# Kernel optimization log

Hardware: AMD Instinct MI355X
Metric: run time of the kernel (lower is better)

## Reference

```python
import jax, jax.numpy as jnp
import numpy as np

T, H, I = 4096, 4096, 11008  # tokens, hidden_size, intermediate_size
QMAX = 127.0


def setup_inputs() -> dict:
    key = jax.random.key(0)
    k0, k1, k2, k3, k4 = jax.random.split(key, 5)
    x = jax.random.normal(k0, (T, H), dtype=jnp.float32)
    # int8 weights stored as float32 integer values in [-127, 127]
    wq_gate_up = jnp.round(jnp.clip(jax.random.normal(k1, (2 * I, H), dtype=jnp.float32) * 30.0, -QMAX, QMAX))
    s_gate_up = jax.random.uniform(k2, (2 * I,), dtype=jnp.float32, minval=5e-4, maxval=2e-3)
    wq_down = jnp.round(jnp.clip(jax.random.normal(k3, (H, I), dtype=jnp.float32) * 30.0, -QMAX, QMAX))
    s_down = jax.random.uniform(k4, (H,), dtype=jnp.float32, minval=5e-4, maxval=2e-3)
    return {"x": x, "wq_gate_up": wq_gate_up, "s_gate_up": s_gate_up,
            "wq_down": wq_down, "s_down": s_down}


def reference(x, wq_gate_up, s_gate_up, wq_down, s_down):
    # --- quantize activations (per-tensor dynamic int8) ---
    x_scale = jnp.max(jnp.abs(x)) / QMAX
    qx = jnp.clip(jnp.round(x / x_scale), -QMAX, QMAX)  # integer-valued f32 (simulated int8)

    # --- gate_up_proj: int8 GEMM (int32 accumulate simulated in f32) ---
    acc = qx @ wq_gate_up.T                             # [T, 2I]
    gate_up = acc * (x_scale * s_gate_up)               # dequant: per-tensor act * per-channel weight scale

    # --- DequantSiluAndMulQuant: silu(gate) * up, then dynamic requant ---
    gate, up = jnp.split(gate_up, 2, axis=-1)           # [T, I] each
    h = jax.nn.silu(gate) * up
    h_scale = jnp.max(jnp.abs(h)) / QMAX
    qh = jnp.clip(jnp.round(h / h_scale), -QMAX, QMAX)

    # --- down_proj: int8 GEMM + dequant ---
    out = (qh @ wq_down.T) * (h_scale * s_down)         # [T, H]
    return out, h_scale
```

## Files before the change

kernel.cpp:

```cpp
#include <hip/hip_runtime.h>

#define T_DIM 4096
#define K1    4096
#define I_DIM 11008
#define QMAXF 127.0f

typedef int v4i  __attribute__((ext_vector_type(4)));
typedef int v16i __attribute__((ext_vector_type(16)));


__device__ __forceinline__ void gload16(const void* g, void* l) {
  __builtin_amdgcn_global_load_lds((__attribute__((address_space(1))) unsigned int*)(g),
                                   (__attribute__((address_space(3))) unsigned int*)(l),
                                   16, 0, 0);
}

__device__ __forceinline__ int packq(float a, float b, float c, float d) {
  return ((int)a & 255) | (((int)b & 255) << 8) | (((int)c & 255) << 16) | (((int)d & 255) << 24);
}

#define MFMA32(A, B, C) __builtin_amdgcn_mfma_i32_32x32x32_i8(A, B, C, 0, 0, 0)


__global__ void absmax_x_kernel(const float4* __restrict__ x4, unsigned* __restrict__ maxbits, int n4) {
  int tid = blockIdx.x * blockDim.x + threadIdx.x;
  int stride = gridDim.x * blockDim.x;
  float m = 0.f;
  for (int i = tid; i < n4; i += stride) {
    float4 v = x4[i];
    m = fmaxf(m, fmaxf(fmaxf(fabsf(v.x), fabsf(v.y)), fmaxf(fabsf(v.z), fabsf(v.w))));
  }
  #pragma unroll
  for (int off = 32; off; off >>= 1) m = fmaxf(m, __shfl_xor(m, off));
  if ((threadIdx.x & 63) == 0) atomicMax(maxbits, __float_as_uint(m));
}


__global__ void quant_x_kernel(const float4* __restrict__ x4, v4i* __restrict__ q4,
                               const unsigned* __restrict__ scal) {
  const float sx = __uint_as_float(scal[0]) * (1.0f / QMAXF);
  const long i = (long)blockIdx.x * blockDim.x + threadIdx.x;
  v4i o;
  #pragma unroll
  for (int j = 0; j < 4; ++j) {
    float4 v = x4[i * 4 + j];
    float a = fminf(fmaxf(rintf(v.x / sx), -QMAXF), QMAXF);
    float b = fminf(fmaxf(rintf(v.y / sx), -QMAXF), QMAXF);
    float c = fminf(fmaxf(rintf(v.z / sx), -QMAXF), QMAXF);
    float d = fminf(fmaxf(rintf(v.w / sx), -QMAXF), QMAXF);
    o[j] = packq(a, b, c, d);
  }
  q4[i] = o;
}


__global__ void conv_w_kernel(const float4* __restrict__ w4, v4i* __restrict__ q4) {
  const long i = (long)blockIdx.x * blockDim.x + threadIdx.x;
  v4i o;
  #pragma unroll
  for (int j = 0; j < 4; ++j) {
    float4 v = w4[i * 4 + j];
    o[j] = packq(rintf(v.x), rintf(v.y), rintf(v.z), rintf(v.w));
  }
  q4[i] = o;
}


#define STG2(KO, SB) {                                                      \
    gload16(gAs + (KO),      &L[SB][lA]);                                   \
    gload16(gAs + (KO) + 32, &L[SB][lA + 8192]);                            \
    gload16(gBs + (KO),      &L[SB][lB]);                                   \
    gload16(gBs + (KO) + 32, &L[SB][lB + 8192]);                            \
  }

#define WBODY(U)                                                            \
  {                                                                         \
    const signed char* Lb = L[(U)];                                         \
    v4i a0 = *(const v4i*)&Lb[kgl * 4096 + ab];                             \
    v4i a1 = *(const v4i*)&Lb[kgl * 4096 + ab + 512];                       \
    v4i b0 = *(const v4i*)&Lb[kgl * 4096 + bb];                             \
    v4i b1 = *(const v4i*)&Lb[kgl * 4096 + bb + 512];                       \
    v4i b2 = *(const v4i*)&Lb[kgl * 4096 + bb + 1024];                      \
    v4i b3 = *(const v4i*)&Lb[kgl * 4096 + bb + 1536];                      \
    v4i a2 = *(const v4i*)&Lb[(2 + kgl) * 4096 + ab];                       \
    v4i a3 = *(const v4i*)&Lb[(2 + kgl) * 4096 + ab + 512];                 \
    v4i b4 = *(const v4i*)&Lb[(2 + kgl) * 4096 + bb];                       \
    v4i b5 = *(const v4i*)&Lb[(2 + kgl) * 4096 + bb + 512];                 \
    v4i b6 = *(const v4i*)&Lb[(2 + kgl) * 4096 + bb + 1024];                \
    v4i b7 = *(const v4i*)&Lb[(2 + kgl) * 4096 + bb + 1536];                \
    acc[0][0] = MFMA32(a0, b0, acc[0][0]);                                  \
    acc[0][1] = MFMA32(a0, b1, acc[0][1]);                                  \
    acc[0][2] = MFMA32(a0, b2, acc[0][2]);                                  \
    acc[0][3] = MFMA32(a0, b3, acc[0][3]);                                  \
    acc[1][0] = MFMA32(a1, b0, acc[1][0]);                                  \
    acc[1][1] = MFMA32(a1, b1, acc[1][1]);                                  \
    acc[1][2] = MFMA32(a1, b2, acc[1][2]);                                  \
    acc[1][3] = MFMA32(a1, b3, acc[1][3]);                                  \
    acc[0][0] = MFMA32(a2, b4, acc[0][0]);                                  \
    acc[0][1] = MFMA32(a2, b5, acc[0][1]);                                  \
    acc[0][2] = MFMA32(a2, b6, acc[0][2]);                                  \
    acc[0][3] = MFMA32(a2, b7, acc[0][3]);                                  \
    acc[1][0] = MFMA32(a3, b4, acc[1][0]);                                  \
    acc[1][1] = MFMA32(a3, b5, acc[1][1]);                                  \
    acc[1][2] = MFMA32(a3, b6, acc[1][2]);                                  \
    acc[1][3] = MFMA32(a3, b7, acc[1][3]);                                  \
  }

#define WINDOW(U0, U1, S0, S1, KO0, KO1, DS0, DS1)                          \
  {                                                                         \
    asm volatile("s_waitcnt vmcnt(0)" ::: "memory");                        \
    __builtin_amdgcn_s_barrier();                                           \
    asm volatile("" ::: "memory");                                          \
    if (DS0) STG2(KO0, S0);                                                 \
    if (DS1) STG2(KO1, S1);                                                 \
    WBODY(U0)                                                               \
    WBODY(U1)                                                               \
  }


__global__ __launch_bounds__(512, 2)
void gemm1_silu_kernel(const signed char* __restrict__ qx,
                       const signed char* __restrict__ w8,
                       const float* __restrict__ sgu,
                       unsigned* __restrict__ scal,
                       float* __restrict__ hbuf)
{
  __shared__ signed char L[4][32768];

  const int tid  = threadIdx.x;
  const int lane = tid & 63;
  const int wid  = tid >> 6;
  const int wr   = wid >> 1;
  const int wc   = wid & 1;
  const int l31  = lane & 31;
  const int kgl  = lane >> 5;

  const int lin = blockIdx.x;
  const int sw  = (lin & 7) * 172 + (lin >> 3);
  const int brow = (sw & 15) * 256;
  const int bcol = (sw >> 4) * 128;

  const int sr = tid & 255, sk = tid >> 8;
  const signed char* gA = qx + (size_t)(brow + sr) * K1 + sk * 16;
  const int grp = sr >> 6, w = sr & 63;
  const int gcolw = bcol + grp * 32 + (w & 31);
  const size_t srcrow = (w < 32) ? (size_t)gcolw : (size_t)(I_DIM + gcolw);
  const signed char* gB = w8 + srcrow * K1 + sk * 16;
  const int lA = tid * 16;
  const int lB = 16384 + tid * 16;

  const int ab = (wr * 64 + l31) * 16;
  const int bb = 16384 + (wc * 128 + l31) * 16;

  v16i zero = {0};
  v16i acc[2][4];
  #pragma unroll
  for (int m = 0; m < 2; ++m)
    #pragma unroll
    for (int n = 0; n < 4; ++n) acc[m][n] = zero;

  const signed char* gAs = gA;
  const signed char* gBs = gB;

  STG2(0, 0);
  STG2(64, 1);

  for (int p = 0; p < 15; ++p) {
    WINDOW(0, 1, 2, 3, 128, 192, 1, 1)
    WINDOW(2, 3, 0, 1, 256, 320, 1, 1)
    gAs += 256; gBs += 256;
  }
  WINDOW(0, 1, 2, 3, 128, 192, 1, 1)
  WINDOW(2, 3, 0, 1, 0, 0, 0, 0)

  const float xsc = __uint_as_float(scal[0]) * (1.0f / QMAXF);
  float hmax = 0.f;
  #pragma unroll
  for (int m = 0; m < 2; ++m) {
    const int rbase = brow + wr * 64 + m * 32 + 4 * kgl;
    #pragma unroll
    for (int p = 0; p < 2; ++p) {
      const int col = bcol + (wc * 2 + p) * 32 + l31;
      const float sg = sgu[col] * xsc;
      const float su = sgu[I_DIM + col] * xsc;
      #pragma unroll
      for (int q = 0; q < 16; ++q) {
        const int row = rbase + (q & 3) + 8 * (q >> 2);
        float g = (float)acc[m][2 * p][q] * sg;
        float u = (float)acc[m][2 * p + 1][q] * su;
        float hv = (g / (1.f + expf(-g))) * u;
        hmax = fmaxf(hmax, fabsf(hv));
        hbuf[(size_t)row * I_DIM + col] = hv;
      }
    }
  }
  #pragma unroll
  for (int off = 32; off; off >>= 1) hmax = fmaxf(hmax, __shfl_xor(hmax, off));
  if (lane == 0) atomicMax(scal + 1, __float_as_uint(hmax));
}


__global__ void quant_h_kernel(const float4* __restrict__ h4, v4i* __restrict__ q4,
                               const unsigned* __restrict__ scal, float* __restrict__ hs_out) {
  const float hs = __uint_as_float(scal[1]) * (1.0f / QMAXF);
  const long i = (long)blockIdx.x * blockDim.x + threadIdx.x;
  if (i == 0) hs_out[0] = hs;
  v4i o;
  #pragma unroll
  for (int j = 0; j < 4; ++j) {
    float4 v = h4[i * 4 + j];
    float a = fminf(fmaxf(rintf(v.x / hs), -QMAXF), QMAXF);
    float b = fminf(fmaxf(rintf(v.y / hs), -QMAXF), QMAXF);
    float c = fminf(fmaxf(rintf(v.z / hs), -QMAXF), QMAXF);
    float d = fminf(fmaxf(rintf(v.w / hs), -QMAXF), QMAXF);
    o[j] = packq(a, b, c, d);
  }
  q4[i] = o;
}


__global__ __launch_bounds__(512, 2)
void gemm2_kernel(const signed char* __restrict__ qh,
                  const signed char* __restrict__ w8,
                  const float* __restrict__ sdn,
                  const unsigned* __restrict__ scal,
                  float* __restrict__ out)
{
  __shared__ signed char L[4][32768];

  const int tid  = threadIdx.x;
  const int lane = tid & 63;
  const int wid  = tid >> 6;
  const int wr   = wid >> 1;
  const int wc   = wid & 1;
  const int l31  = lane & 31;
  const int kgl  = lane >> 5;

  const int lin = blockIdx.x;
  const int sw  = (lin & 7) * 32 + (lin >> 3);
  const int brow = (sw & 15) * 256;
  const int bcol = (sw >> 4) * 256;

  const int sr = tid & 255, sk = tid >> 8;
  const signed char* gA = qh + (size_t)(brow + sr) * I_DIM + sk * 16;
  const signed char* gB = w8 + (size_t)(bcol + sr) * I_DIM + sk * 16;
  const int lA = tid * 16;
  const int lB = 16384 + tid * 16;

  const int ab = (wr * 64 + l31) * 16;
  const int bb = 16384 + (wc * 128 + l31) * 16;

  v16i zero = {0};
  v16i acc[2][4];
  #pragma unroll
  for (int m = 0; m < 2; ++m)
    #pragma unroll
    for (int n = 0; n < 4; ++n) acc[m][n] = zero;

  const signed char* gAs = gA;
  const signed char* gBs = gB;

  STG2(0, 0);
  STG2(64, 1);

  for (int p = 0; p < 42; ++p) {
    WINDOW(0, 1, 2, 3, 128, 192, 1, 1)
    WINDOW(2, 3, 0, 1, 256, 320, 1, 1)
    gAs += 256; gBs += 256;
  }
  WINDOW(0, 1, 2, 3, 128, 192, 1, 1)
  WINDOW(2, 3, 0, 1, 0, 0, 0, 0)

  const float hsc = __uint_as_float(scal[1]) * (1.0f / QMAXF);
  #pragma unroll
  for (int m = 0; m < 2; ++m) {
    const int rbase = brow + wr * 64 + m * 32 + 4 * kgl;
    #pragma unroll
    for (int n = 0; n < 4; ++n) {
      const int col = bcol + wc * 128 + n * 32 + l31;
      const float s = sdn[col] * hsc;
      #pragma unroll
      for (int q = 0; q < 16; ++q) {
        const int row = rbase + (q & 3) + 8 * (q >> 2);
        out[(size_t)row * K1 + col] = (float)acc[m][n][q] * s;
      }
    }
  }
}


extern "C" void kernel_launch(void* const* d_in, const int* in_sizes, int n_in,
                              void* d_out, int out_size, void* d_ws, size_t ws_size,
                              hipStream_t stream) {
  (void)in_sizes; (void)n_in; (void)out_size; (void)ws_size;
  const float* x   = (const float*)d_in[0];
  const float* wgu = (const float*)d_in[1];
  const float* sgu = (const float*)d_in[2];
  const float* wdn = (const float*)d_in[3];
  const float* sdn = (const float*)d_in[4];
  float* out = (float*)d_out;
  char* ws = (char*)d_ws;

  signed char* qx  = (signed char*)(ws + 0LL);
  signed char* w8g = (signed char*)(ws + 16777216LL);
  signed char* w8d = (signed char*)(ws + 106954752LL);
  signed char* qh  = (signed char*)(ws + 152043520LL);
  float*       hb  = (float*)      (ws + 197132288LL);
  unsigned*    scal= (unsigned*)   (ws + 377487360LL);

  hipMemsetAsync(scal, 0, 256, stream);
  absmax_x_kernel<<<2048, 256, 0, stream>>>((const float4*)x, scal, T_DIM * K1 / 4);
  quant_x_kernel<<<4096, 256, 0, stream>>>((const float4*)x, (v4i*)qx, scal);
  conv_w_kernel<<<22016, 256, 0, stream>>>((const float4*)wgu, (v4i*)w8g);
  conv_w_kernel<<<11008, 256, 0, stream>>>((const float4*)wdn, (v4i*)w8d);

  gemm1_silu_kernel<<<1376, 512, 0, stream>>>(qx, w8g, sgu, scal, hb);

  quant_h_kernel<<<11008, 256, 0, stream>>>((const float4*)hb, (v4i*)qh, scal,
                                            out + (size_t)T_DIM * K1);

  gemm2_kernel<<<256, 512, 0, stream>>>(qh, w8d, sdn, scal, out);
}
```

Measured before the change: 1.331 ms.

## Shrink GEMM block tiles to 128 rows with triple-buffered LDS pipeline

Both int8 GEMMs drop from 256-row block tiles to 128-row tiles, with 8 waves arranged 2x4 and each wave holding four accumulators instead of eight. The LDS ring goes from four 32 KB stages to three 24 KB stages, and the wait changes from vmcnt(0) to vmcnt(3) so one stage stays in flight while another is consumed. Launch bounds rise to 4 blocks per CU and the grids double. The aim is more resident waves and better load/compute overlap, and gemm2 in particular gets more blocks than CUs. The cost is less operand reuse per block, so more global/L2 traffic per FLOP.

```diff
diff --git a/kernel.cpp b/kernel.cpp
--- a/kernel.cpp
+++ b/kernel.cpp
@@ -66,132 +66,107 @@
 }
 
 
-#define STG2(KO, SB) {                                                      \
-    gload16(gAs + (KO),      &L[SB][lA]);                                   \
-    gload16(gAs + (KO) + 32, &L[SB][lA + 8192]);                            \
-    gload16(gBs + (KO),      &L[SB][lB]);                                   \
-    gload16(gBs + (KO) + 32, &L[SB][lB + 8192]);                            \
-  }
-
-#define WBODY(U)                                                            \
+#define STG3(KO, SB) {                                                      \
+    gload16(gA1 + (KO),      &L[SB][lA]);                                   \
+    gload16(gB1 + (KO),      &L[SB][lB]);                                   \
+    gload16(gB1 + (KO) + 32, &L[SB][lB + 8192]);                            \
+  }
+
+#define TILE(U, SB, KO, DOST, VM)                                           \
   {                                                                         \
+    asm volatile("s_waitcnt vmcnt(" VM ")" ::: "memory");                   \
+    __builtin_amdgcn_s_barrier();                                           \
+    asm volatile("" ::: "memory");                                          \
+    if (DOST) STG3(KO, SB);                                                 \
     const signed char* Lb = L[(U)];                                         \
-    v4i a0 = *(const v4i*)&Lb[kgl * 4096 + ab];                             \
-    v4i a1 = *(const v4i*)&Lb[kgl * 4096 + ab + 512];                       \
+    v4i a0 = *(const v4i*)&Lb[kgl * 2048 + ab];                             \
+    v4i a1 = *(const v4i*)&Lb[kgl * 2048 + ab + 512];                       \
     v4i b0 = *(const v4i*)&Lb[kgl * 4096 + bb];                             \
     v4i b1 = *(const v4i*)&Lb[kgl * 4096 + bb + 512];                       \
-    v4i b2 = *(const v4i*)&Lb[kgl * 4096 + bb + 1024];                      \
-    v4i b3 = *(const v4i*)&Lb[kgl * 4096 + bb + 1536];                      \
-    v4i a2 = *(const v4i*)&Lb[(2 + kgl) * 4096 + ab];                       \
-    v4i a3 = *(const v4i*)&Lb[(2 + kgl) * 4096 + ab + 512];                 \
-    v4i b4 = *(const v4i*)&Lb[(2 + kgl) * 4096 + bb];                       \
-    v4i b5 = *(const v4i*)&Lb[(2 + kgl) * 4096 + bb + 512];                 \
-    v4i b6 = *(const v4i*)&Lb[(2 + kgl) * 4096 + bb + 1024];                \
-    v4i b7 = *(const v4i*)&Lb[(2 + kgl) * 4096 + bb + 1536];                \
-    acc[0][0] = MFMA32(a0, b0, acc[0][0]);                                  \
-    acc[0][1] = MFMA32(a0, b1, acc[0][1]);                                  \
-    acc[0][2] = MFMA32(a0, b2, acc[0][2]);                                  \
-    acc[0][3] = MFMA32(a0, b3, acc[0][3]);                                  \
-    acc[1][0] = MFMA32(a1, b0, acc[1][0]);                                  \
-    acc[1][1] = MFMA32(a1, b1, acc[1][1]);                                  \
-    acc[1][2] = MFMA32(a1, b2, acc[1][2]);                                  \
-    acc[1][3] = MFMA32(a1, b3, acc[1][3]);                                  \
-    acc[0][0] = MFMA32(a2, b4, acc[0][0]);                                  \
-    acc[0][1] = MFMA32(a2, b5, acc[0][1]);                                  \
-    acc[0][2] = MFMA32(a2, b6, acc[0][2]);                                  \
-    acc[0][3] = MFMA32(a2, b7, acc[0][3]);                                  \
-    acc[1][0] = MFMA32(a3, b4, acc[1][0]);                                  \
-    acc[1][1] = MFMA32(a3, b5, acc[1][1]);                                  \
-    acc[1][2] = MFMA32(a3, b6, acc[1][2]);                                  \
-    acc[1][3] = MFMA32(a3, b7, acc[1][3]);                                  \
-  }
-
-#define WINDOW(U0, U1, S0, S1, KO0, KO1, DS0, DS1)                          \
-  {                                                                         \
-    asm volatile("s_waitcnt vmcnt(0)" ::: "memory");                        \
-    __builtin_amdgcn_s_barrier();                                           \
-    asm volatile("" ::: "memory");                                          \
-    if (DS0) STG2(KO0, S0);                                                 \
-    if (DS1) STG2(KO1, S1);                                                 \
-    WBODY(U0)                                                               \
-    WBODY(U1)                                                               \
-  }
-
-
-__global__ __launch_bounds__(512, 2)
+    v4i a2 = *(const v4i*)&Lb[(2 + kgl) * 2048 + ab];                       \
+    v4i a3 = *(const v4i*)&Lb[(2 + kgl) * 2048 + ab + 512];                 \
+    v4i b2 = *(const v4i*)&Lb[(2 + kgl) * 4096 + bb];                       \
+    v4i b3 = *(const v4i*)&Lb[(2 + kgl) * 4096 + bb + 512];                 \
+    acc00 = MFMA32(a0, b0, acc00);                                          \
+    acc01 = MFMA32(a0, b1, acc01);                                          \
+    acc10 = MFMA32(a1, b0, acc10);                                          \
+    acc11 = MFMA32(a1, b1, acc11);                                          \
+    acc00 = MFMA32(a2, b2, acc00);                                          \
+    acc01 = MFMA32(a2, b3, acc01);                                          \
+    acc10 = MFMA32(a3, b2, acc10);                                          \
+    acc11 = MFMA32(a3, b3, acc11);                                          \
+  }
+
+
+__global__ __launch_bounds__(512, 4)
 void gemm1_silu_kernel(const signed char* __restrict__ qx,
                        const signed char* __restrict__ w8,
                        const float* __restrict__ sgu,
                        unsigned* __restrict__ scal,
                        float* __restrict__ hbuf)
 {
-  __shared__ signed char L[4][32768];
+  __shared__ signed char L[3][24576];
 
   const int tid  = threadIdx.x;
   const int lane = tid & 63;
   const int wid  = tid >> 6;
-  const int wr   = wid >> 1;
-  const int wc   = wid & 1;
+  const int wr   = wid >> 2;
+  const int wc   = wid & 3;
   const int l31  = lane & 31;
   const int kgl  = lane >> 5;
 
   const int lin = blockIdx.x;
-  const int sw  = (lin & 7) * 172 + (lin >> 3);
-  const int brow = (sw & 15) * 256;
-  const int bcol = (sw >> 4) * 128;
-
+  const int sw  = (lin & 7) * 344 + (lin >> 3);
+  const int brow = (sw & 31) * 128;
+  const int bcol = (sw >> 5) * 128;
+
+  const int sra = tid & 127, ska = tid >> 7;
+  const signed char* gA1 = qx + (size_t)(brow + sra) * K1 + ska * 16;
   const int sr = tid & 255, sk = tid >> 8;
-  const signed char* gA = qx + (size_t)(brow + sr) * K1 + sk * 16;
   const int grp = sr >> 6, w = sr & 63;
   const int gcolw = bcol + grp * 32 + (w & 31);
   const size_t srcrow = (w < 32) ? (size_t)gcolw : (size_t)(I_DIM + gcolw);
-  const signed char* gB = w8 + srcrow * K1 + sk * 16;
+  const signed char* gB1 = w8 + srcrow * K1 + sk * 16;
   const int lA = tid * 16;
-  const int lB = 16384 + tid * 16;
+  const int lB = 8192 + tid * 16;
 
   const int ab = (wr * 64 + l31) * 16;
-  const int bb = 16384 + (wc * 128 + l31) * 16;
-
-  v16i zero = {0};
-  v16i acc[2][4];
-  #pragma unroll
-  for (int m = 0; m < 2; ++m)
-    #pragma unroll
-    for (int n = 0; n < 4; ++n) acc[m][n] = zero;
-
-  const signed char* gAs = gA;
-  const signed char* gBs = gB;
-
-  STG2(0, 0);
-  STG2(64, 1);
-
-  for (int p = 0; p < 15; ++p) {
-    WINDOW(0, 1, 2, 3, 128, 192, 1, 1)
-    WINDOW(2, 3, 0, 1, 256, 320, 1, 1)
-    gAs += 256; gBs += 256;
-  }
-  WINDOW(0, 1, 2, 3, 128, 192, 1, 1)
-  WINDOW(2, 3, 0, 1, 0, 0, 0, 0)
+  const int bb = 8192 + (wc * 64 + l31) * 16;
+
+  v16i acc00 = {0}, acc01 = {0}, acc10 = {0}, acc11 = {0};
+
+  STG3(0, 0);
+  STG3(64, 1);
+
+  for (int p = 0; p < 20; ++p) {
+    TILE(0, 2, 128, 1, "3")
+    TILE(1, 0, 192, 1, "3")
+    TILE(2, 1, 256, 1, "3")
+    gA1 += 192; gB1 += 192;
+  }
+  TILE(0, 2, 128, 1, "3")
+  TILE(1, 0, 192, 1, "3")
+  TILE(2, 0, 0,   0, "3")
+  TILE(0, 0, 0,   0, "0")
 
   const float xsc = __uint_as_float(scal[0]) * (1.0f / QMAXF);
+  const int col = bcol + wc * 32 + l31;
+  const float sg = sgu[col] * xsc;
+  const float su = sgu[I_DIM + col] * xsc;
   float hmax = 0.f;
   #pragma unroll
   for (int m = 0; m < 2; ++m) {
     const int rbase = brow + wr * 64 + m * 32 + 4 * kgl;
+    const v16i ag = m ? acc10 : acc00;
+    const v16i au = m ? acc11 : acc01;
     #pragma unroll
-    for (int p = 0; p < 2; ++p) {
-      const int col = bcol + (wc * 2 + p) * 32 + l31;
-      const float sg = sgu[col] * xsc;
-      const float su = sgu[I_DIM + col] * xsc;
-      #pragma unroll
-      for (int q = 0; q < 16; ++q) {
-        const int row = rbase + (q & 3) + 8 * (q >> 2);
-        float g = (float)acc[m][2 * p][q] * sg;
-        float u = (float)acc[m][2 * p + 1][q] * su;
-        float hv = (g / (1.f + expf(-g))) * u;
-        hmax = fmaxf(hmax, fabsf(hv));
-        hbuf[(size_t)row * I_DIM + col] = hv;
-      }
+    for (int q = 0; q < 16; ++q) {
+      const int row = rbase + (q & 3) + 8 * (q >> 2);
+      float g = (float)ag[q] * sg;
+      float u = (float)au[q] * su;
+      float hv = (g / (1.f + expf(-g))) * u;
+      hmax = fmaxf(hmax, fabsf(hv));
+      hbuf[(size_t)row * I_DIM + col] = hv;
     }
   }
   #pragma unroll
@@ -219,70 +194,67 @@
 }
 
 
-__global__ __launch_bounds__(512, 2)
+__global__ __launch_bounds__(512, 4)
 void gemm2_kernel(const signed char* __restrict__ qh,
                   const signed char* __restrict__ w8,
                   const float* __restrict__ sdn,
                   const unsigned* __restrict__ scal,
                   float* __restrict__ out)
 {
-  __shared__ signed char L[4][32768];
+  __shared__ signed char L[3][24576];
 
   const int tid  = threadIdx.x;
   const int lane = tid & 63;
   const int wid  = tid >> 6;
-  const int wr   = wid >> 1;
-  const int wc   = wid & 1;
+  const int wr   = wid >> 2;
+  const int wc   = wid & 3;
   const int l31  = lane & 31;
   const int kgl  = lane >> 5;
 
   const int lin = blockIdx.x;
-  const int sw  = (lin & 7) * 32 + (lin >> 3);
-  const int brow = (sw & 15) * 256;
-  const int bcol = (sw >> 4) * 256;
-
+  const int sw  = (lin & 7) * 64 + (lin >> 3);
+  const int brow = (sw & 31) * 128;
+  const int bcol = (sw >> 5) * 256;
+
+  const int sra = tid & 127, ska = tid >> 7;
+  const signed char* gA1 = qh + (size_t)(brow + sra) * I_DIM + ska * 16;
   const int sr = tid & 255, sk = tid >> 8;
-  const signed char* gA = qh + (size_t)(brow + sr) * I_DIM + sk * 16;
-  const signed char* gB = w8 + (size_t)(bcol + sr) * I_DIM + sk * 16;
+  const signed char* gB1 = w8 + (size_t)(bcol + sr) * I_DIM + sk * 16;
   const int lA = tid * 16;
-  const int lB = 16384 + tid * 16;
+  const int lB = 8192 + tid * 16;
 
   const int ab = (wr * 64 + l31) * 16;
-  const int bb = 16384 + (wc * 128 + l31) * 16;
-
-  v16i zero = {0};
-  v16i acc[2][4];
-  #pragma unroll
-  for (int m = 0; m < 2; ++m)
-    #pragma unroll
-    for (int n = 0; n < 4; ++n) acc[m][n] = zero;
-
-  const signed char* gAs = gA;
-  const signed char* gBs = gB;
-
-  STG2(0, 0);
-  STG2(64, 1);
-
-  for (int p = 0; p < 42; ++p) {
-    WINDOW(0, 1, 2, 3, 128, 192, 1, 1)
-    WINDOW(2, 3, 0, 1, 256, 320, 1, 1)
-    gAs += 256; gBs += 256;
-  }
-  WINDOW(0, 1, 2, 3, 128, 192, 1, 1)
-  WINDOW(2, 3, 0, 1, 0, 0, 0, 0)
+  const int bb = 8192 + (wc * 64 + l31) * 16;
+
+  v16i acc00 = {0}, acc01 = {0}, acc10 = {0}, acc11 = {0};
+
+  STG3(0, 0);
+  STG3(64, 1);
+
+  for (int p = 0; p < 56; ++p) {
+    TILE(0, 2, 128, 1, "3")
+    TILE(1, 0, 192, 1, "3")
+    TILE(2, 1, 256, 1, "3")
+    gA1 += 192; gB1 += 192;
+  }
+  TILE(0, 2, 128, 1, "3")
+  TILE(1, 0, 192, 1, "3")
+  TILE(2, 0, 0,   0, "3")
+  TILE(0, 0, 0,   0, "0")
 
   const float hsc = __uint_as_float(scal[1]) * (1.0f / QMAXF);
   #pragma unroll
   for (int m = 0; m < 2; ++m) {
     const int rbase = brow + wr * 64 + m * 32 + 4 * kgl;
     #pragma unroll
-    for (int n = 0; n < 4; ++n) {
-      const int col = bcol + wc * 128 + n * 32 + l31;
+    for (int n = 0; n < 2; ++n) {
+      const int col = bcol + wc * 64 + n * 32 + l31;
       const float s = sdn[col] * hsc;
+      const v16i av = m ? (n ? acc11 : acc10) : (n ? acc01 : acc00);
       #pragma unroll
       for (int q = 0; q < 16; ++q) {
         const int row = rbase + (q & 3) + 8 * (q >> 2);
-        out[(size_t)row * K1 + col] = (float)acc[m][n][q] * s;
+        out[(size_t)row * K1 + col] = (float)av[q] * s;
       }
     }
   }
@@ -314,10 +286,10 @@
   conv_w_kernel<<<22016, 256, 0, stream>>>((const float4*)wgu, (v4i*)w8g);
   conv_w_kernel<<<11008, 256, 0, stream>>>((const float4*)wdn, (v4i*)w8d);
 
-  gemm1_silu_kernel<<<1376, 512, 0, stream>>>(qx, w8g, sgu, scal, hb);
+  gemm1_silu_kernel<<<2752, 512, 0, stream>>>(qx, w8g, sgu, scal, hb);
 
   quant_h_kernel<<<11008, 256, 0, stream>>>((const float4*)hb, (v4i*)qh, scal,
                                             out + (size_t)T_DIM * K1);
 
-  gemm2_kernel<<<256, 512, 0, stream>>>(qh, w8d, sdn, scal, out);
-}
+  gemm2_kernel<<<512, 512, 0, stream>>>(qh, w8d, sdn, scal, out);
+}
```

New measurement: 1.535 ms. 15.4% more time.

## Restructure int8 GEMM main loops into double-buffered two-phase pipeline with priority hints

Applied to the files above, without the earlier changes.

Both GEMM kernels replace the four-slot 64-wide K staging with two 128-wide K buffers, so each iteration has one vmcnt wait and barrier instead of two. Each iteration is split into two phases: LDS fragments are read first, then the A half or B half of the next tile is issued, then a barrier and lgkmcnt wait precede the MFMA burst. The MFMA burst is raised with s_setprio and fenced by sched_barrier. The aim is to interleave global-to-LDS loads with matrix math and cut synchronisation overhead. The trade-off is a shallower prefetch depth (one tile ahead), which may expose memory latency.

```diff
diff --git a/kernel.cpp b/kernel.cpp
--- a/kernel.cpp
+++ b/kernel.cpp
@@ -66,55 +66,68 @@
 }
 
 
-#define STG2(KO, SB) {                                                      \
-    gload16(gAs + (KO),      &L[SB][lA]);                                   \
-    gload16(gAs + (KO) + 32, &L[SB][lA + 8192]);                            \
-    gload16(gBs + (KO),      &L[SB][lB]);                                   \
-    gload16(gBs + (KO) + 32, &L[SB][lB + 8192]);                            \
-  }
-
-#define WBODY(U)                                                            \
+#define STG_A4(KO, LS) {                                                    \
+    gload16(gA + (KO),      &LS[lA]);                                       \
+    gload16(gA + (KO) + 32, &LS[lA + 8192]);                                \
+    gload16(gA + (KO) + 64, &LS[lA + 16384]);                               \
+    gload16(gA + (KO) + 96, &LS[lA + 24576]);                               \
+  }
+#define STG_B4(KO, LS) {                                                    \
+    gload16(gB + (KO),      &LS[lB]);                                       \
+    gload16(gB + (KO) + 32, &LS[lB + 8192]);                                \
+    gload16(gB + (KO) + 64, &LS[lB + 16384]);                               \
+    gload16(gB + (KO) + 96, &LS[lB + 24576]);                               \
+  }
+
+#define PHASE(KS0, STMT_STAGE)                                              \
   {                                                                         \
-    const signed char* Lb = L[(U)];                                         \
-    v4i a0 = *(const v4i*)&Lb[kgl * 4096 + ab];                             \
-    v4i a1 = *(const v4i*)&Lb[kgl * 4096 + ab + 512];                       \
-    v4i b0 = *(const v4i*)&Lb[kgl * 4096 + bb];                             \
-    v4i b1 = *(const v4i*)&Lb[kgl * 4096 + bb + 512];                       \
-    v4i b2 = *(const v4i*)&Lb[kgl * 4096 + bb + 1024];                      \
-    v4i b3 = *(const v4i*)&Lb[kgl * 4096 + bb + 1536];                      \
-    v4i a2 = *(const v4i*)&Lb[(2 + kgl) * 4096 + ab];                       \
-    v4i a3 = *(const v4i*)&Lb[(2 + kgl) * 4096 + ab + 512];                 \
-    v4i b4 = *(const v4i*)&Lb[(2 + kgl) * 4096 + bb];                       \
-    v4i b5 = *(const v4i*)&Lb[(2 + kgl) * 4096 + bb + 512];                 \
-    v4i b6 = *(const v4i*)&Lb[(2 + kgl) * 4096 + bb + 1024];                \
-    v4i b7 = *(const v4i*)&Lb[(2 + kgl) * 4096 + bb + 1536];                \
-    acc[0][0] = MFMA32(a0, b0, acc[0][0]);                                  \
-    acc[0][1] = MFMA32(a0, b1, acc[0][1]);                                  \
-    acc[0][2] = MFMA32(a0, b2, acc[0][2]);                                  \
-    acc[0][3] = MFMA32(a0, b3, acc[0][3]);                                  \
-    acc[1][0] = MFMA32(a1, b0, acc[1][0]);                                  \
-    acc[1][1] = MFMA32(a1, b1, acc[1][1]);                                  \
-    acc[1][2] = MFMA32(a1, b2, acc[1][2]);                                  \
-    acc[1][3] = MFMA32(a1, b3, acc[1][3]);                                  \
-    acc[0][0] = MFMA32(a2, b4, acc[0][0]);                                  \
-    acc[0][1] = MFMA32(a2, b5, acc[0][1]);                                  \
-    acc[0][2] = MFMA32(a2, b6, acc[0][2]);                                  \
-    acc[0][3] = MFMA32(a2, b7, acc[0][3]);                                  \
-    acc[1][0] = MFMA32(a3, b4, acc[1][0]);                                  \
-    acc[1][1] = MFMA32(a3, b5, acc[1][1]);                                  \
-    acc[1][2] = MFMA32(a3, b6, acc[1][2]);                                  \
-    acc[1][3] = MFMA32(a3, b7, acc[1][3]);                                  \
-  }
-
-#define WINDOW(U0, U1, S0, S1, KO0, KO1, DS0, DS1)                          \
-  {                                                                         \
+    v4i a00 = *(const v4i*)&Lb[(KS0 + kgl) * 4096 + ab];                    \
+    v4i a01 = *(const v4i*)&Lb[(KS0 + kgl) * 4096 + ab + 512];              \
+    v4i b00 = *(const v4i*)&Lb[(KS0 + kgl) * 4096 + bb];                    \
+    v4i b01 = *(const v4i*)&Lb[(KS0 + kgl) * 4096 + bb + 512];              \
+    v4i b02 = *(const v4i*)&Lb[(KS0 + kgl) * 4096 + bb + 1024];             \
+    v4i b03 = *(const v4i*)&Lb[(KS0 + kgl) * 4096 + bb + 1536];             \
+    v4i a10 = *(const v4i*)&Lb[(KS0 + 2 + kgl) * 4096 + ab];                \
+    v4i a11 = *(const v4i*)&Lb[(KS0 + 2 + kgl) * 4096 + ab + 512];          \
+    v4i b10 = *(const v4i*)&Lb[(KS0 + 2 + kgl) * 4096 + bb];                \
+    v4i b11 = *(const v4i*)&Lb[(KS0 + 2 + kgl) * 4096 + bb + 512];          \
+    v4i b12 = *(const v4i*)&Lb[(KS0 + 2 + kgl) * 4096 + bb + 1024];         \
+    v4i b13 = *(const v4i*)&Lb[(KS0 + 2 + kgl) * 4096 + bb + 1536];         \
+    STMT_STAGE                                                              \
+    __builtin_amdgcn_s_barrier();                                           \
+    asm volatile("s_waitcnt lgkmcnt(0)" ::: "memory");                      \
+    __builtin_amdgcn_sched_barrier(0);                                      \
+    __builtin_amdgcn_s_setprio(1);                                          \
+    acc[0][0] = MFMA32(a00, b00, acc[0][0]);                                \
+    acc[0][1] = MFMA32(a00, b01, acc[0][1]);                                \
+    acc[0][2] = MFMA32(a00, b02, acc[0][2]);                                \
+    acc[0][3] = MFMA32(a00, b03, acc[0][3]);                                \
+    acc[1][0] = MFMA32(a01, b00, acc[1][0]);                                \
+    acc[1][1] = MFMA32(a01, b01, acc[1][1]);                                \
+    acc[1][2] = MFMA32(a01, b02, acc[1][2]);                                \
+    acc[1][3] = MFMA32(a01, b03, acc[1][3]);                                \
+    acc[0][0] = MFMA32(a10, b10, acc[0][0]);                                \
+    acc[0][1] = MFMA32(a10, b11, acc[0][1]);                                \
+    acc[0][2] = MFMA32(a10, b12, acc[0][2]);                                \
+    acc[0][3] = MFMA32(a10, b13, acc[0][3]);                                \
+    acc[1][0] = MFMA32(a11, b10, acc[1][0]);                                \
+    acc[1][1] = MFMA32(a11, b11, acc[1][1]);                                \
+    acc[1][2] = MFMA32(a11, b12, acc[1][2]);                                \
+    acc[1][3] = MFMA32(a11, b13, acc[1][3]);                                \
+    __builtin_amdgcn_s_setprio(0);                                          \
+  }
+
+#define KLOOP(NK)                                                           \
+  for (int t = 0; t < (NK); ++t) {                                          \
     asm volatile("s_waitcnt vmcnt(0)" ::: "memory");                        \
     __builtin_amdgcn_s_barrier();                                           \
     asm volatile("" ::: "memory");                                          \
-    if (DS0) STG2(KO0, S0);                                                 \
-    if (DS1) STG2(KO1, S1);                                                 \
-    WBODY(U0)                                                               \
-    WBODY(U1)                                                               \
+    const signed char* Lb = L[t & 1];                                       \
+    signed char* Ls = L[(t + 1) & 1];                                       \
+    const bool st = (t + 1) < (NK);                                         \
+    const int ko = (t + 1) * 128;                                           \
+    PHASE(0, if (st) STG_A4(ko, Ls))                                        \
+    PHASE(4, if (st) STG_B4(ko, Ls))                                        \
   }
 
 
@@ -125,7 +138,7 @@
                        unsigned* __restrict__ scal,
                        float* __restrict__ hbuf)
 {
-  __shared__ signed char L[4][32768];
+  __shared__ signed char L[2][65536];
 
   const int tid  = threadIdx.x;
   const int lane = tid & 63;
@@ -147,10 +160,10 @@
   const size_t srcrow = (w < 32) ? (size_t)gcolw : (size_t)(I_DIM + gcolw);
   const signed char* gB = w8 + srcrow * K1 + sk * 16;
   const int lA = tid * 16;
-  const int lB = 16384 + tid * 16;
+  const int lB = 32768 + tid * 16;
 
   const int ab = (wr * 64 + l31) * 16;
-  const int bb = 16384 + (wc * 128 + l31) * 16;
+  const int bb = 32768 + (wc * 128 + l31) * 16;
 
   v16i zero = {0};
   v16i acc[2][4];
@@ -159,19 +172,11 @@
     #pragma unroll
     for (int n = 0; n < 4; ++n) acc[m][n] = zero;
 
-  const signed char* gAs = gA;
-  const signed char* gBs = gB;
-
-  STG2(0, 0);
-  STG2(64, 1);
-
-  for (int p = 0; p < 15; ++p) {
-    WINDOW(0, 1, 2, 3, 128, 192, 1, 1)
-    WINDOW(2, 3, 0, 1, 256, 320, 1, 1)
-    gAs += 256; gBs += 256;
-  }
-  WINDOW(0, 1, 2, 3, 128, 192, 1, 1)
-  WINDOW(2, 3, 0, 1, 0, 0, 0, 0)
+  const int nk = K1 / 128;
+  STG_A4(0, L[0]);
+  STG_B4(0, L[0]);
+
+  KLOOP(nk)
 
   const float xsc = __uint_as_float(scal[0]) * (1.0f / QMAXF);
   float hmax = 0.f;
@@ -226,7 +231,7 @@
                   const unsigned* __restrict__ scal,
                   float* __restrict__ out)
 {
-  __shared__ signed char L[4][32768];
+  __shared__ signed char L[2][65536];
 
   const int tid  = threadIdx.x;
   const int lane = tid & 63;
@@ -245,10 +250,10 @@
   const signed char* gA = qh + (size_t)(brow + sr) * I_DIM + sk * 16;
   const signed char* gB = w8 + (size_t)(bcol + sr) * I_DIM + sk * 16;
   const int lA = tid * 16;
-  const int lB = 16384 + tid * 16;
+  const int lB = 32768 + tid * 16;
 
   const int ab = (wr * 64 + l31) * 16;
-  const int bb = 16384 + (wc * 128 + l31) * 16;
+  const int bb = 32768 + (wc * 128 + l31) * 16;
 
   v16i zero = {0};
   v16i acc[2][4];
@@ -257,19 +262,11 @@
     #pragma unroll
     for (int n = 0; n < 4; ++n) acc[m][n] = zero;
 
-  const signed char* gAs = gA;
-  const signed char* gBs = gB;
-
-  STG2(0, 0);
-  STG2(64, 1);
-
-  for (int p = 0; p < 42; ++p) {
-    WINDOW(0, 1, 2, 3, 128, 192, 1, 1)
-    WINDOW(2, 3, 0, 1, 256, 320, 1, 1)
-    gAs += 256; gBs += 256;
-  }
-  WINDOW(0, 1, 2, 3, 128, 192, 1, 1)
-  WINDOW(2, 3, 0, 1, 0, 0, 0, 0)
+  const int nk = I_DIM / 128;
+  STG_A4(0, L[0]);
+  STG_B4(0, L[0]);
+
+  KLOOP(nk)
 
   const float hsc = __uint_as_float(scal[1]) * (1.0f / QMAXF);
   #pragma unroll
```

Result: faster. 1.173 ms (-11.8%).
